# Optimization experiments

Hardware: AMD Instinct MI355X
Metric: run time of the kernel (lower is better)

## Reference

```python
import jax, jax.numpy as jnp
import numpy as np

THRESH = 0.5
MARGIN = 0.1
SCALE_POS = 2.0
SCALE_NEG = 40.0
EPSILON = 1e-5


def setup_inputs() -> dict:
    key = jax.random.key(0)
    kx, kl = jax.random.split(key)
    B, D, N_CLASSES = 4096, 1024, 256
    x = jax.random.normal(kx, (B, D), dtype=jnp.float32)
    # L2-normalize embeddings (standard for multi-similarity loss; keeps sim in [-1, 1])
    x = x / jnp.linalg.norm(x, axis=1, keepdims=True)
    labels = jax.random.randint(kl, (B,), 0, N_CLASSES, dtype=jnp.int64)
    return {"x": x, "labels": labels}


def reference(x, labels):
    B = x.shape[0]
    sim = jnp.matmul(x, x.T)  # [B, B]

    eye = jnp.eye(B, dtype=bool)
    same = labels[:, None] == labels[None, :]
    pos_mask = same & ~eye                      # positives excl. self
    neg_mask = ~same                            # negatives
    pos_valid = pos_mask & (sim < 1.0 - EPSILON)  # pos_pair_ after < 1-eps filter

    # per-row hardest stats (inf/-inf where empty)
    min_pos = jnp.min(jnp.where(pos_valid, sim, jnp.inf), axis=1)   # min over pos_pair_
    max_neg = jnp.max(jnp.where(neg_mask, sim, -jnp.inf), axis=1)   # max over neg_pair_

    # mined pairs
    neg_keep = neg_mask & (sim + MARGIN > min_pos[:, None])
    pos_keep = pos_valid & (sim - MARGIN < max_neg[:, None])

    has_row = (pos_valid.any(axis=1) & neg_mask.any(axis=1)
               & pos_keep.any(axis=1) & neg_keep.any(axis=1))

    pos_sum = jnp.sum(jnp.where(pos_keep, jnp.exp(-SCALE_POS * (sim - THRESH)), 0.0), axis=1)
    neg_sum = jnp.sum(jnp.where(neg_keep, jnp.exp(SCALE_NEG * (sim - THRESH)), 0.0), axis=1)

    pos_loss = jnp.log1p(pos_sum) / SCALE_POS
    neg_loss = jnp.log1p(neg_sum) / SCALE_NEG

    row_loss = jnp.where(has_row, pos_loss + neg_loss, 0.0)
    return jnp.sum(row_loss) / B
```

## Files before the change

### kernel.cpp

```cpp
#include <hip/hip_runtime.h>
#include <hip/hip_bf16.h>
#include <math.h>
#include <stdint.h>


#define THRESH    0.5f
#define MARGIN    0.1f
#define SCALE_POS 2.0f
#define SCALE_NEG 40.0f
#define POS_CAP   (1.0f - 1e-5f)

typedef __bf16 bf16x8 __attribute__((ext_vector_type(8)));
typedef float  f32x4  __attribute__((ext_vector_type(4)));

__device__ __forceinline__ uint16_t f2bf(float f) {
  union { float f; uint32_t u; } v; v.f = f;
  uint32_t u = v.u;
  u += 0x7FFFu + ((u >> 16) & 1u);
  return (uint16_t)(u >> 16);
}

__device__ __forceinline__ uint32_t fenc(float f) {
  union { float f; uint32_t u; } v; v.f = f;
  return (v.u & 0x80000000u) ? ~v.u : (v.u ^ 0x80000000u);
}
__device__ __forceinline__ float fdec(uint32_t k) {
  union { float f; uint32_t u; } v;
  v.u = (k & 0x80000000u) ? (k ^ 0x80000000u) : ~k;
  return v.f;
}

__global__ __launch_bounds__(256) void cvt_bf16_kernel(
    const float* __restrict__ x, uint16_t* __restrict__ y, int n) {
  int i = (blockIdx.x * 256 + threadIdx.x) * 4;
  if (i + 3 < n) {
    float4 v = *(const float4*)(x + i);
    ushort4 o;
    o.x = f2bf(v.x); o.y = f2bf(v.y); o.z = f2bf(v.z); o.w = f2bf(v.w);
    *(ushort4*)(y + i) = o;
  }
}

#if defined(__has_builtin)
#if __has_builtin(__builtin_amdgcn_global_load_lds)
#define HAVE_GLL 1
#endif
#endif

__device__ __forceinline__ void stage16(const uint16_t* g, uint16_t* lds_wave_base, int lane) {
#ifdef HAVE_GLL
  __builtin_amdgcn_global_load_lds(
      (const __attribute__((address_space(1))) void*)g,
      (__attribute__((address_space(3))) void*)lds_wave_base, 16, 0, 0);
#else
  *(uint4*)(lds_wave_base + lane * 8) = *(const uint4*)g;
#endif
}

__global__ __launch_bounds__(256) void simgemm_kernel(
    const uint16_t* __restrict__ X, const int* __restrict__ labels,
    float* __restrict__ C, uint32_t* __restrict__ gmin, uint32_t* __restrict__ gmax,
    int B, int D) {
  __shared__ __align__(16) uint16_t sA[128 * 32];
  __shared__ __align__(16) uint16_t sB[128 * 32];
  __shared__ int slabR[128];
  __shared__ int slabC[128];

  int t = blockIdx.x;
  const int nblk = B >> 7;
  int bi = 0;
  while (t >= nblk - bi) { t -= nblk - bi; ++bi; }
  const int bj = bi + t;
  const int bm = bi * 128;
  const int bn = bj * 128;

  const int tid  = threadIdx.x;
  const int wave = tid >> 6;
  const int lane = tid & 63;
  const int waveM = wave >> 1, waveN = wave & 1;

  if (tid < 128) slabR[tid] = labels[bm + tid];
  else           slabC[tid - 128] = labels[bn + tid - 128];

  const uint16_t* gA = X + (size_t)bm * D;
  const uint16_t* gB = X + (size_t)bn * D;

  uint16_t* lA0 = sA + wave * 512;
  uint16_t* lA1 = sA + 2048 + wave * 512;
  uint16_t* lB0 = sB + wave * 512;
  uint16_t* lB1 = sB + 2048 + wave * 512;

  const int r0 = tid >> 2,           c0 = (tid & 3) * 8;
  const int r1 = (tid + 256) >> 2,   c1 = (tid & 3) * 8;

  const int fr = lane & 15;
  const int fq = lane >> 4;
  const int aoff = (waveM * 64 + fr) * 32 + fq * 8;
  const int boff = (waveN * 64 + fr) * 32 + fq * 8;

  f32x4 acc[4][4] = {};

  for (int k0 = 0; k0 < D; k0 += 32) {
    stage16(gA + (size_t)r0 * D + k0 + c0, lA0, lane);
    stage16(gA + (size_t)r1 * D + k0 + c1, lA1, lane);
    stage16(gB + (size_t)r0 * D + k0 + c0, lB0, lane);
    stage16(gB + (size_t)r1 * D + k0 + c1, lB1, lane);
    __syncthreads();

    bf16x8 af[4], bfv[4];
#pragma unroll
    for (int tt = 0; tt < 4; ++tt) af[tt]  = *(const bf16x8*)(sA + aoff + tt * 512);
#pragma unroll
    for (int tt = 0; tt < 4; ++tt) bfv[tt] = *(const bf16x8*)(sB + boff + tt * 512);

#pragma unroll
    for (int mt = 0; mt < 4; ++mt)
#pragma unroll
      for (int nt = 0; nt < 4; ++nt)
        acc[mt][nt] = __builtin_amdgcn_mfma_f32_16x16x32_bf16(
            af[mt], bfv[nt], acc[mt][nt], 0, 0, 0);
    __syncthreads();
  }

#pragma unroll
  for (int mt = 0; mt < 4; ++mt) {
#pragma unroll
    for (int nt = 0; nt < 4; ++nt) {
      const int col = bn + waveN * 64 + nt * 16 + fr;
#pragma unroll
      for (int r = 0; r < 4; ++r) {
        const int row = bm + waveM * 64 + mt * 16 + fq * 4 + r;
        C[(size_t)row * B + col] = acc[mt][nt][r];
      }
    }
  }

  if (bi != bj) {
#pragma unroll
    for (int mt = 0; mt < 4; ++mt) {
#pragma unroll
      for (int nt = 0; nt < 4; ++nt) {
        const int col  = bn + waveN * 64 + nt * 16 + fr;
        const int rowb = bm + waveM * 64 + mt * 16 + fq * 4;
        *(f32x4*)(C + (size_t)col * B + rowb) = acc[mt][nt];
      }
    }
  }

  const float INF = __builtin_inff();

  int lr[4][4];
#pragma unroll
  for (int mt = 0; mt < 4; ++mt)
#pragma unroll
    for (int r = 0; r < 4; ++r)
      lr[mt][r] = slabR[waveM * 64 + mt * 16 + fq * 4 + r];
  int lc[4];
#pragma unroll
  for (int nt = 0; nt < 4; ++nt) lc[nt] = slabC[waveN * 64 + nt * 16 + fr];

  {
    float rmin[4][4], rmax[4][4];
#pragma unroll
    for (int mt = 0; mt < 4; ++mt)
#pragma unroll
      for (int r = 0; r < 4; ++r) { rmin[mt][r] = INF; rmax[mt][r] = -INF; }

#pragma unroll
    for (int mt = 0; mt < 4; ++mt) {
#pragma unroll
      for (int nt = 0; nt < 4; ++nt) {
        const int gcol = bn + waveN * 64 + nt * 16 + fr;
#pragma unroll
        for (int r = 0; r < 4; ++r) {
          const int grow = bm + waveM * 64 + mt * 16 + fq * 4 + r;
          const float s = acc[mt][nt][r];
          if (lr[mt][r] == lc[nt]) {
            if (grow != gcol && s < POS_CAP) rmin[mt][r] = fminf(rmin[mt][r], s);
          } else {
            rmax[mt][r] = fmaxf(rmax[mt][r], s);
          }
        }
      }
    }
#pragma unroll
    for (int mt = 0; mt < 4; ++mt)
#pragma unroll
      for (int r = 0; r < 4; ++r) {
#pragma unroll
        for (int m = 1; m < 16; m <<= 1) {
          rmin[mt][r] = fminf(rmin[mt][r], __shfl_xor(rmin[mt][r], m, 64));
          rmax[mt][r] = fmaxf(rmax[mt][r], __shfl_xor(rmax[mt][r], m, 64));
        }
      }
    if (fr == 0) {
#pragma unroll
      for (int mt = 0; mt < 4; ++mt)
#pragma unroll
        for (int r = 0; r < 4; ++r) {
          const int grow = bm + waveM * 64 + mt * 16 + fq * 4 + r;
          if (rmin[mt][r] < INF)  atomicMin(&gmin[grow], fenc(rmin[mt][r]));
          if (rmax[mt][r] > -INF) atomicMax(&gmax[grow], fenc(rmax[mt][r]));
        }
    }
  }

  if (bi != bj) {
    float cmin[4], cmax[4];
#pragma unroll
    for (int nt = 0; nt < 4; ++nt) { cmin[nt] = INF; cmax[nt] = -INF; }

#pragma unroll
    for (int nt = 0; nt < 4; ++nt) {
      const int gcol = bn + waveN * 64 + nt * 16 + fr;
#pragma unroll
      for (int mt = 0; mt < 4; ++mt) {
#pragma unroll
        for (int r = 0; r < 4; ++r) {
          const int grow = bm + waveM * 64 + mt * 16 + fq * 4 + r;
          const float s = acc[mt][nt][r];
          if (lc[nt] == lr[mt][r]) {
            if (grow != gcol && s < POS_CAP) cmin[nt] = fminf(cmin[nt], s);
          } else {
            cmax[nt] = fmaxf(cmax[nt], s);
          }
        }
      }
    }
#pragma unroll
    for (int nt = 0; nt < 4; ++nt) {
#pragma unroll
      for (int m = 16; m < 64; m <<= 1) {
        cmin[nt] = fminf(cmin[nt], __shfl_xor(cmin[nt], m, 64));
        cmax[nt] = fmaxf(cmax[nt], __shfl_xor(cmax[nt], m, 64));
      }
    }
    if (fq == 0) {
#pragma unroll
      for (int nt = 0; nt < 4; ++nt) {
        const int gcol = bn + waveN * 64 + nt * 16 + fr;
        if (cmin[nt] < INF)  atomicMin(&gmin[gcol], fenc(cmin[nt]));
        if (cmax[nt] > -INF) atomicMax(&gmax[gcol], fenc(cmax[nt]));
      }
    }
  }
}

__global__ __launch_bounds__(256) void rowloss_kernel(
    const float* __restrict__ sim, const int* __restrict__ labels,
    const uint32_t* __restrict__ gmin, const uint32_t* __restrict__ gmax,
    float* __restrict__ rowbuf, int B) {
  __shared__ int   slab[4096];
  __shared__ float red[8];

  const int tid  = threadIdx.x;
  const int wave = tid >> 6;
  const int lane = tid & 63;
  const float INF = __builtin_inff();

  for (int tq = tid; tq < (B >> 2); tq += 256)
    ((int4*)slab)[tq] = ((const int4*)labels)[tq];
  __syncthreads();

  const int iters = B >> 10;
  for (int rr = 0; rr < 4; ++rr) {
    const int i = blockIdx.x * 4 + rr;
    const float* row = sim + (size_t)i * B;
    const int li = slab[i];

    const uint32_t kmin = gmin[i], kmax = gmax[i];
    const bool haspos = (kmin != 0xFFFFFFFFu);
    const bool hasneg = (kmax != 0u);
    const float minpos = haspos ? fdec(kmin) : INF;
    const float maxneg = hasneg ? fdec(kmax) : -INF;

    float psum = 0.f, nsum = 0.f;
    for (int it = 0; it < iters; ++it) {
      const int j = it * 1024 + tid * 4;
      float4 v = *(const float4*)(row + j);
      float s4[4] = {v.x, v.y, v.z, v.w};
#pragma unroll
      for (int q = 0; q < 4; ++q) {
        const int jj = j + q;
        const float s = s4[q];
        if (slab[jj] == li) {
          if (jj != i && s < POS_CAP && (s - MARGIN < maxneg))
            psum += __expf(-SCALE_POS * (s - THRESH));
        } else {
          if (s + MARGIN > minpos)
            nsum += __expf(SCALE_NEG * (s - THRESH));
        }
      }
    }

#pragma unroll
    for (int m = 32; m > 0; m >>= 1) {
      psum += __shfl_xor(psum, m, 64);
      nsum += __shfl_xor(nsum, m, 64);
    }
    if (lane == 0) { red[wave] = psum; red[4 + wave] = nsum; }
    __syncthreads();

    if (tid == 0) {
      psum = red[0] + red[1] + red[2] + red[3];
      nsum = red[4] + red[5] + red[6] + red[7];
      const bool has_row = haspos && hasneg && (psum > 0.f) && (nsum > 0.f);
      rowbuf[i] = has_row
          ? (log1pf(psum) * (1.0f / SCALE_POS) + log1pf(nsum) * (1.0f / SCALE_NEG))
          : 0.f;
    }
    __syncthreads();
  }
}

__global__ __launch_bounds__(256) void finalreduce_kernel(
    const float* __restrict__ rowbuf, float* __restrict__ out, int B) {
  __shared__ float red[4];
  const int tid  = threadIdx.x;
  const int wave = tid >> 6;
  const int lane = tid & 63;

  float s = 0.f;
  for (int j = tid * 4; j < B; j += 1024) {
    float4 v = *(const float4*)(rowbuf + j);
    s += v.x + v.y + v.z + v.w;
  }
#pragma unroll
  for (int m = 32; m > 0; m >>= 1) s += __shfl_xor(s, m, 64);
  if (lane == 0) red[wave] = s;
  __syncthreads();
  if (tid == 0)
    out[0] = (red[0] + red[1] + red[2] + red[3]) * (1.0f / (float)B);
}

extern "C" void kernel_launch(void* const* d_in, const int* in_sizes, int n_in,
                              void* d_out, int out_size, void* d_ws, size_t ws_size,
                              hipStream_t stream) {
  const float* x      = (const float*)d_in[0];
  const int*   labels = (const int*)d_in[1];
  float*       out    = (float*)d_out;

  const int B = in_sizes[1];
  const int D = in_sizes[0] / B;

  uint16_t* xbf = (uint16_t*)d_ws;
  size_t xbytes = (((size_t)B * D * 2) + 255) & ~(size_t)255;
  float* sim = (float*)((char*)d_ws + xbytes);
  size_t simbytes = (size_t)B * B * 4;
  float* rowbuf = (float*)((char*)d_ws + xbytes + simbytes);
  uint32_t* gmin = (uint32_t*)((char*)d_ws + xbytes + simbytes + (size_t)B * 4);
  uint32_t* gmax = (uint32_t*)((char*)d_ws + xbytes + simbytes + (size_t)B * 8);

  hipMemsetAsync(gmin, 0xFF, (size_t)B * 4, stream);
  hipMemsetAsync(gmax, 0x00, (size_t)B * 4, stream);

  const int n = B * D;
  cvt_bf16_kernel<<<n / 1024, 256, 0, stream>>>(x, xbf, n);

  const int nblk = B / 128;
  const int nb   = nblk * (nblk + 1) / 2;
  simgemm_kernel<<<nb, 256, 0, stream>>>(xbf, labels, sim, gmin, gmax, B, D);

  rowloss_kernel<<<B / 4, 256, 0, stream>>>(sim, labels, gmin, gmax, rowbuf, B);
  finalreduce_kernel<<<1, 256, 0, stream>>>(rowbuf, out, B);
}
```

Measured before the change: 159.5 us.

## Double-buffer swizzled 64-wide K tiles and remap blocks across XCDs in sim GEMM

The K-loop of the similarity GEMM now stages 64-wide K tiles into two LDS buffers. The next tile's global-to-LDS loads are issued while MFMAs run on the current tile, with one barrier per iteration instead of two. An XOR swizzle on the LDS layout is meant to cut bank conflicts on the fragment reads. Block indices are also permuted so that contiguous triangular tiles land on the same XCD for better L2 reuse. In exchange, LDS use rises to 64 KB per block, which may limit occupancy.

```diff
diff --git a/kernel.cpp b/kernel.cpp
--- a/kernel.cpp
+++ b/kernel.cpp
@@ -61,13 +61,18 @@
     const uint16_t* __restrict__ X, const int* __restrict__ labels,
     float* __restrict__ C, uint32_t* __restrict__ gmin, uint32_t* __restrict__ gmax,
     int B, int D) {
-  __shared__ __align__(16) uint16_t sA[128 * 32];
-  __shared__ __align__(16) uint16_t sB[128 * 32];
+  __shared__ __align__(16) uint16_t sT[2][2][128 * 64];
   __shared__ int slabR[128];
   __shared__ int slabC[128];
 
+  const int nblk = B >> 7;
+  const int nb   = nblk * (nblk + 1) / 2;
+
   int t = blockIdx.x;
-  const int nblk = B >> 7;
+  if ((nb & 7) == 0) {
+    const int cpx = nb >> 3;
+    t = (t % 8) * cpx + t / 8;
+  }
   int bi = 0;
   while (t >= nblk - bi) { t -= nblk - bi; ++bi; }
   const int bj = bi + t;
@@ -85,41 +90,71 @@
   const uint16_t* gA = X + (size_t)bm * D;
   const uint16_t* gB = X + (size_t)bn * D;
 
-  uint16_t* lA0 = sA + wave * 512;
-  uint16_t* lA1 = sA + 2048 + wave * 512;
-  uint16_t* lB0 = sB + wave * 512;
-  uint16_t* lB1 = sB + 2048 + wave * 512;
-
-  const int r0 = tid >> 2,           c0 = (tid & 3) * 8;
-  const int r1 = (tid + 256) >> 2,   c1 = (tid & 3) * 8;
+  int srcOff[4];
+#pragma unroll
+  for (int s = 0; s < 4; ++s) {
+    const int idx = s * 256 + tid;
+    const int row = idx >> 3;
+    const int cb  = ((idx & 7) << 4) ^ ((row & 7) << 4);
+    srcOff[s] = row * D + (cb >> 1);
+  }
 
   const int fr = lane & 15;
   const int fq = lane >> 4;
-  const int aoff = (waveM * 64 + fr) * 32 + fq * 8;
-  const int boff = (waveN * 64 + fr) * 32 + fq * 8;
+  const int sw = (fr & 7) << 4;
 
   f32x4 acc[4][4] = {};
 
-  for (int k0 = 0; k0 < D; k0 += 32) {
-    stage16(gA + (size_t)r0 * D + k0 + c0, lA0, lane);
-    stage16(gA + (size_t)r1 * D + k0 + c1, lA1, lane);
-    stage16(gB + (size_t)r0 * D + k0 + c0, lB0, lane);
-    stage16(gB + (size_t)r1 * D + k0 + c1, lB1, lane);
+  const int NT = D >> 6;
+
+#pragma unroll
+  for (int s = 0; s < 4; ++s) {
+    uint16_t* dA = &sT[0][0][0] + (s * 256 + wave * 64) * 8;
+    uint16_t* dB = &sT[0][1][0] + (s * 256 + wave * 64) * 8;
+    stage16(gA + srcOff[s], dA, lane);
+    stage16(gB + srcOff[s], dB, lane);
+  }
+  __syncthreads();
+
+  int cur = 0;
+  for (int kt = 0; kt < NT; ++kt) {
+    if (kt + 1 < NT) {
+      const int k0 = (kt + 1) << 6;
+#pragma unroll
+      for (int s = 0; s < 4; ++s) {
+        uint16_t* dA = &sT[cur ^ 1][0][0] + (s * 256 + wave * 64) * 8;
+        uint16_t* dB = &sT[cur ^ 1][1][0] + (s * 256 + wave * 64) * 8;
+        stage16(gA + srcOff[s] + k0, dA, lane);
+        stage16(gB + srcOff[s] + k0, dB, lane);
+      }
+    }
+
+    const char* tA = (const char*)&sT[cur][0][0];
+    const char* tB = (const char*)&sT[cur][1][0];
+#pragma unroll
+    for (int kk = 0; kk < 2; ++kk) {
+      const int cbyte = (kk * 64 + fq * 16) ^ sw;
+      bf16x8 af[4], bfv[4];
+#pragma unroll
+      for (int mt = 0; mt < 4; ++mt) {
+        const int rowa = waveM * 64 + mt * 16 + fr;
+        af[mt] = *(const bf16x8*)(tA + rowa * 128 + cbyte);
+      }
+#pragma unroll
+      for (int nt = 0; nt < 4; ++nt) {
+        const int rowb = waveN * 64 + nt * 16 + fr;
+        bfv[nt] = *(const bf16x8*)(tB + rowb * 128 + cbyte);
+      }
+#pragma unroll
+      for (int mt = 0; mt < 4; ++mt)
+#pragma unroll
+        for (int nt = 0; nt < 4; ++nt)
+          acc[mt][nt] = __builtin_amdgcn_mfma_f32_16x16x32_bf16(
+              af[mt], bfv[nt], acc[mt][nt], 0, 0, 0);
+    }
+
     __syncthreads();
-
-    bf16x8 af[4], bfv[4];
-#pragma unroll
-    for (int tt = 0; tt < 4; ++tt) af[tt]  = *(const bf16x8*)(sA + aoff + tt * 512);
-#pragma unroll
-    for (int tt = 0; tt < 4; ++tt) bfv[tt] = *(const bf16x8*)(sB + boff + tt * 512);
-
-#pragma unroll
-    for (int mt = 0; mt < 4; ++mt)
-#pragma unroll
-      for (int nt = 0; nt < 4; ++nt)
-        acc[mt][nt] = __builtin_amdgcn_mfma_f32_16x16x32_bf16(
-            af[mt], bfv[nt], acc[mt][nt], 0, 0, 0);
-    __syncthreads();
+    cur ^= 1;
   }
 
 #pragma unroll
```

Measured after the change: 148.1 us. 1.08x faster.
